# Kernel tuning notes

Hardware: AMD Instinct MI355X
Metric: run time of the kernel (lower is better)

The kernel has to match this reference:

```python
import jax, jax.numpy as jnp
import numpy as np

N_NODES = 50000
N_EDGES = 800000
D_IN, D_HID, D_OUT = 96, 96, 48


def _gcn_conv(x, src, dst, W, b, num_nodes):
    """PyG GCNConv: h = x @ W; out[dst] += norm * h[src]; out += b.
    Symmetric normalization deg^{-1/2}[src] * deg^{-1/2}[dst], self-loops included
    (src/dst already contain self-loops)."""
    h = x @ W  # [N, d_out]
    deg = jax.ops.segment_sum(jnp.ones_like(dst, dtype=h.dtype), dst,
                              num_segments=num_nodes)  # in-degree incl. self-loop
    dinv = jnp.where(deg > 0, jax.lax.rsqrt(deg), 0.0)
    norm = dinv[src] * dinv[dst]  # [E+N]
    msgs = h[src] * norm[:, None]  # gather + scale (the memory-bound part)
    out = jax.ops.segment_sum(msgs, dst, num_segments=num_nodes)  # scatter-add
    return out + b


def setup_inputs() -> dict:
    key = jax.random.key(0)
    k1, k2, k3, k4 = jax.random.split(key, 4)
    x = jax.random.normal(k1, (N_NODES, D_IN), dtype=jnp.float32)
    edge_index = jax.random.randint(k2, (2, N_EDGES), 0, N_NODES, dtype=jnp.int64)
    # Glorot-ish init for weights, zero bias (matches GCNConv defaults)
    W1 = jax.random.normal(k3, (D_IN, D_HID), dtype=jnp.float32) / np.sqrt(D_IN)
    b1 = jnp.zeros((D_HID,), dtype=jnp.float32)
    W2 = jax.random.normal(k4, (D_HID, D_OUT), dtype=jnp.float32) / np.sqrt(D_HID)
    b2 = jnp.zeros((D_OUT,), dtype=jnp.float32)
    return {"x": x, "edge_index": edge_index, "W1": W1, "b1": b1, "W2": W2, "b2": b2}


def reference(x, edge_index, W1, b1, W2, b2):
    num_nodes = x.shape[0]
    loops = jnp.arange(num_nodes, dtype=edge_index.dtype)
    src = jnp.concatenate([edge_index[0], loops])  # add self-loops
    dst = jnp.concatenate([edge_index[1], loops])
    h = _gcn_conv(x, src, dst, W1, b1, num_nodes)
    h = jax.nn.relu(h)
    # dropout p=0.5 is identity in eval mode (self.training=False)
    out = _gcn_conv(h, src, dst, W2, b2, num_nodes)
    return out
```

## Files before the change

kernel.cpp:

```cpp
#include <hip/hip_runtime.h>
#include <hip/hip_bf16.h>


constexpr int NN = 50000;
constexpr int NE = 800000;
constexpr int DI = 96;
constexpr int DH = 96;
constexpr int DO = 48;

constexpr int BK_SHIFT = 6;
constexpr int NBK      = (NN + 63) >> 6;
constexpr int BK_CAP   = 2048;

constexpr int NCHUNK = 256;
constexpr int CH     = (NE + NCHUNK - 1) / NCHUNK;

typedef unsigned short us8 __attribute__((ext_vector_type(8)));

__device__ __forceinline__ float bf2f(unsigned short u) {
    return __uint_as_float(((unsigned int)u) << 16);
}
__device__ __forceinline__ unsigned short f2bf(float f) {
    __hip_bfloat16 b = __float2bfloat16(f);
    return *reinterpret_cast<unsigned short*>(&b);
}


__global__ __launch_bounds__(256) void k_hist(const int* __restrict__ dst,
                                              int* __restrict__ C, int e) {
    __shared__ int hist[NBK];
    for (int i = threadIdx.x; i < NBK; i += 256) hist[i] = 0;
    __syncthreads();
    const int blk = blockIdx.x;
    const int beg = blk * CH, end = min(beg + CH, e);
    for (int i = beg + threadIdx.x; i < end; i += 256)
        atomicAdd(&hist[dst[i] >> BK_SHIFT], 1);
    __syncthreads();
    for (int b = threadIdx.x; b < NBK; b += 256)
        C[b * NCHUNK + blk] = hist[b];
}

__global__ __launch_bounds__(256) void k_rowscan(int* __restrict__ C,
                                                 int* __restrict__ totals,
                                                 int* __restrict__ row_ptr) {
    if (blockIdx.x == 0 && threadIdx.x == 0) row_ptr[NN] = NE;
    const int w    = threadIdx.x >> 6;
    const int lane = threadIdx.x & 63;
    const int r    = blockIdx.x * 4 + w;
    if (r >= NBK) return;
    int* row = C + r * NCHUNK;
    int v[4], s[4];
#pragma unroll
    for (int q = 0; q < 4; ++q) { v[q] = row[q * 64 + lane]; s[q] = v[q]; }
#pragma unroll
    for (int off = 1; off < 64; off <<= 1) {
#pragma unroll
        for (int q = 0; q < 4; ++q) {
            int y = __shfl_up(s[q], off);
            if (lane >= off) s[q] += y;
        }
    }
    int c0 = __shfl(s[0], 63);
    int c1 = __shfl(s[1], 63);
    int c2 = __shfl(s[2], 63);
    s[1] += c0;
    s[2] += c0 + c1;
    s[3] += c0 + c1 + c2;
#pragma unroll
    for (int q = 0; q < 4; ++q) row[q * 64 + lane] = s[q] - v[q];
    if (lane == 63) totals[r] = s[3];
}

__global__ __launch_bounds__(256) void k_scatter(const int* __restrict__ src,
                                                 const int* __restrict__ dst,
                                                 const int* __restrict__ C,
                                                 const int* __restrict__ totals,
                                                 int* __restrict__ bk_ptr,
                                                 unsigned* __restrict__ ebuf, int e) {
    __shared__ int bkL[NBK + 1];
    __shared__ int part[256];
    __shared__ int cur[NBK];
    const int t = threadIdx.x;

    int v[4];
    int s = 0;
    const int base = t * 4;
#pragma unroll
    for (int i = 0; i < 4; ++i) {
        int idx = base + i;
        v[i] = (idx < NBK) ? totals[idx] : 0;
        s += v[i];
    }
    part[t] = s;
    __syncthreads();
#pragma unroll
    for (int off = 1; off < 256; off <<= 1) {
        int x = part[t];
        int a = (t >= off) ? part[t - off] : 0;
        __syncthreads();
        part[t] = x + a;
        __syncthreads();
    }
    int run = part[t] - s;
#pragma unroll
    for (int i = 0; i < 4; ++i) {
        int idx = base + i;
        if (idx <= NBK) bkL[idx] = run;
        run += v[i];
    }
    __syncthreads();

    const int blk = blockIdx.x;
    for (int b = t; b < NBK; b += 256) cur[b] = bkL[b] + C[b * NCHUNK + blk];
    if (blk == 0)
        for (int i = t; i <= NBK; i += 256) bk_ptr[i] = bkL[i];
    __syncthreads();

    const int beg = blk * CH, end = min(beg + CH, e);
    for (int i = beg + t; i < end; i += 256) {
        int d = dst[i];
        int b = d >> BK_SHIFT;
        int pos = atomicAdd(&cur[b], 1);
        ebuf[pos] = ((unsigned)(d & 63) << 16) | (unsigned)src[i];
    }
}

__global__ __launch_bounds__(256) void k_bsort(const unsigned* __restrict__ ebuf,
                                               const int* __restrict__ bk_ptr,
                                               int* __restrict__ row_ptr,
                                               float* __restrict__ dinv,
                                               unsigned short* __restrict__ src16, int n) {
    __shared__ unsigned eL[BK_CAP];
    __shared__ unsigned short outL[BK_CAP];
    __shared__ int curL[64];
    __shared__ int baseL[64];

    const int b   = blockIdx.x;
    const int beg = bk_ptr[b];
    const int m   = bk_ptr[b + 1] - beg;
    const int t   = threadIdx.x;

    if (t < 64) curL[t] = 0;
    __syncthreads();

    for (int i = t; i < m; i += 256) {
        unsigned v = ebuf[beg + i];
        eL[i] = v;
        atomicAdd(&curL[v >> 16], 1);
    }
    __syncthreads();

    if (t < 64) {
        int c = curL[t];
        int x = c;
#pragma unroll
        for (int off = 1; off < 64; off <<= 1) {
            int y = __shfl_up(x, off);
            if (t >= off) x += y;
        }
        int excl = x - c;
        baseL[t] = excl;
        int d0 = (b << BK_SHIFT) + t;
        if (d0 < n) {
            row_ptr[d0] = beg + excl;
            dinv[d0]    = rsqrtf((float)(c + 1));
        }
    }
    __syncthreads();
    if (t < 64) curL[t] = baseL[t];
    __syncthreads();

    for (int i = t; i < m; i += 256) {
        unsigned v = eL[i];
        int p = atomicAdd(&curL[v >> 16], 1);
        outL[p] = (unsigned short)(v & 0xFFFFu);
    }
    __syncthreads();
    for (int i = t; i < m; i += 256) src16[beg + i] = outL[i];
}


__global__ __launch_bounds__(256) void k_gemm1(const float* __restrict__ X,
                                               const float* __restrict__ W,
                                               const float* __restrict__ dinv,
                                               unsigned short* __restrict__ Hsl, int n) {
    constexpr int ROWS = 64, P = 97;
    __shared__ float ws[DI * DH];
    __shared__ float xs[ROWS * P];
    unsigned short* hout = reinterpret_cast<unsigned short*>(xs);

    const int tid  = threadIdx.x;
    const int row0 = blockIdx.x * ROWS;

    for (int i = tid; i < DI * DH; i += 256) ws[i] = W[i];
    {
        const float4* Xv = reinterpret_cast<const float4*>(X + (size_t)row0 * DI);
        const int nv   = ROWS * DI / 4;
        const int maxv = ((n - row0) * DI) / 4;
        for (int i = tid; i < nv; i += 256) {
            float4 v = (i < maxv) ? Xv[i] : float4{0.f, 0.f, 0.f, 0.f};
            int r = i / 24, c = (i % 24) * 4;
            xs[r * P + c + 0] = v.x;
            xs[r * P + c + 1] = v.y;
            xs[r * P + c + 2] = v.z;
            xs[r * P + c + 3] = v.w;
        }
    }
    __syncthreads();

    const int cg = tid & 15, rg = tid >> 4;
    float acc[4][6] = {};
#pragma unroll 2
    for (int k = 0; k < DI; ++k) {
        float xv[4];
#pragma unroll
        for (int i = 0; i < 4; ++i) xv[i] = xs[(rg * 4 + i) * P + k];
#pragma unroll
        for (int j = 0; j < 6; ++j) {
            float wv = ws[k * DH + cg * 6 + j];
#pragma unroll
            for (int i = 0; i < 4; ++i) acc[i][j] += xv[i] * wv;
        }
    }
    __syncthreads();

#pragma unroll
    for (int i = 0; i < 4; ++i) {
        int row = row0 + rg * 4 + i;
        float dv = (row < n) ? dinv[row] : 0.f;
#pragma unroll
        for (int j = 0; j < 6; ++j)
            hout[(rg * 4 + i) * 96 + cg * 6 + j] = f2bf(acc[i][j] * dv);
    }
    __syncthreads();

    if (tid < 192) {
        int s = tid >> 6, r = tid & 63;
        int row = row0 + r;
        if (row < n) {
            const us8* srcp = reinterpret_cast<const us8*>(hout + r * 96 + s * 32);
            us8* dstp = reinterpret_cast<us8*>(Hsl + ((size_t)s * n + row) * 32);
#pragma unroll
            for (int q = 0; q < 4; ++q) dstp[q] = srcp[q];
        }
    }
}


__global__ __launch_bounds__(256) void k_gemm2(const unsigned short* __restrict__ A,
                                               const float* __restrict__ W,
                                               const float* __restrict__ dinv,
                                               unsigned short* __restrict__ H, int n) {
    constexpr int ROWS = 64, P = 98;
    __shared__ float ws[DH * DO];
    __shared__ unsigned short xs[ROWS * P];

    const int tid  = threadIdx.x;
    const int row0 = blockIdx.x * ROWS;

    for (int i = tid; i < DH * DO; i += 256) ws[i] = W[i];
    {
        const us8* Av = reinterpret_cast<const us8*>(A + (size_t)row0 * DH);
        const int nv   = ROWS * DH / 8;
        const int maxv = ((n - row0) * DH) / 8;
        for (int i = tid; i < nv; i += 256) {
            us8 v = (i < maxv) ? Av[i] : (us8)(0);
            int r = i / 12, c = (i % 12) * 8;
#pragma unroll
            for (int jj = 0; jj < 8; ++jj) xs[r * P + c + jj] = v[jj];
        }
    }
    __syncthreads();

    const int cg = tid & 15, rg = tid >> 4;
    float acc[4][3] = {};
#pragma unroll 2
    for (int k = 0; k < DH; ++k) {
        float xv[4];
#pragma unroll
        for (int i = 0; i < 4; ++i) xv[i] = bf2f(xs[(rg * 4 + i) * P + k]);
#pragma unroll
        for (int j = 0; j < 3; ++j) {
            float wv = ws[k * DO + cg * 3 + j];
#pragma unroll
            for (int i = 0; i < 4; ++i) acc[i][j] += xv[i] * wv;
        }
    }

#pragma unroll
    for (int i = 0; i < 4; ++i) {
        int row = row0 + rg * 4 + i;
        if (row < n) {
            float dv = dinv[row];
#pragma unroll
            for (int j = 0; j < 3; ++j)
                H[(size_t)row * DO + cg * 3 + j] = f2bf(acc[i][j] * dv);
        }
    }
}


__global__ __launch_bounds__(256) void k_agg_sl3(const unsigned short* __restrict__ hsl,
                                                 const float* __restrict__ dinv,
                                                 const int* __restrict__ row_ptr,
                                                 const unsigned short* __restrict__ src16,
                                                 const float* __restrict__ bias,
                                                 unsigned short* __restrict__ a1, int n) {
    const int v   = blockIdx.x & 7;
    const int s   = (v >= 6) ? (v - 6) : (v >= 3 ? v - 3 : v);
    const int rep = (v >= 6) ? 2 : (v >= 3 ? 1 : 0);
    const int R   = (s == 2) ? 2 : 3;
    const int cnt = (n + R - 1) / R;
    const int lo  = rep * cnt;
    const int hi  = min(lo + cnt, n);
    const int node = lo + ((int)(blockIdx.x >> 3) << 6) + ((int)threadIdx.x >> 2);
    if (node >= hi) return;
    const int g = threadIdx.x & 3;

    const us8* hs = reinterpret_cast<const us8*>(hsl + (size_t)s * n * 32);

    float accA[8], accB[8];
    {
        us8 hv = hs[(size_t)node * 4 + g];
#pragma unroll
        for (int j = 0; j < 8; ++j) { accA[j] = bf2f(hv[j]); accB[j] = 0.f; }
    }

    const int beg = row_ptr[node];
    const int end = row_ptr[node + 1];
    int k = beg;
    int kA = min((beg + 7) & ~7, end);
    for (; k < kA; ++k) {
        us8 vv = hs[(size_t)src16[k] * 4 + g];
#pragma unroll
        for (int j = 0; j < 8; ++j) accA[j] += bf2f(vv[j]);
    }
    for (; k + 8 <= end; k += 8) {
        us8 si = *reinterpret_cast<const us8*>(src16 + k);
        us8 v0 = hs[(size_t)si[0] * 4 + g];
        us8 v1 = hs[(size_t)si[1] * 4 + g];
        us8 v2 = hs[(size_t)si[2] * 4 + g];
        us8 v3 = hs[(size_t)si[3] * 4 + g];
        us8 v4 = hs[(size_t)si[4] * 4 + g];
        us8 v5 = hs[(size_t)si[5] * 4 + g];
        us8 v6 = hs[(size_t)si[6] * 4 + g];
        us8 v7 = hs[(size_t)si[7] * 4 + g];
#pragma unroll
        for (int j = 0; j < 8; ++j) {
            accA[j] += (bf2f(v0[j]) + bf2f(v1[j])) + (bf2f(v4[j]) + bf2f(v5[j]));
            accB[j] += (bf2f(v2[j]) + bf2f(v3[j])) + (bf2f(v6[j]) + bf2f(v7[j]));
        }
    }
    for (; k < end; ++k) {
        us8 vv = hs[(size_t)src16[k] * 4 + g];
#pragma unroll
        for (int j = 0; j < 8; ++j) accB[j] += bf2f(vv[j]);
    }

    const float di = dinv[node];
    const float4* b4 = reinterpret_cast<const float4*>(bias);
    float4 b0 = b4[s * 8 + g * 2], b1 = b4[s * 8 + g * 2 + 1];
    float r[8];
#pragma unroll
    for (int j = 0; j < 8; ++j) r[j] = di * (accA[j] + accB[j]);
    r[0] += b0.x; r[1] += b0.y; r[2] += b0.z; r[3] += b0.w;
    r[4] += b1.x; r[5] += b1.y; r[6] += b1.z; r[7] += b1.w;
    us8 o;
#pragma unroll
    for (int j = 0; j < 8; ++j) o[j] = f2bf(fmaxf(r[j], 0.f));
    *reinterpret_cast<us8*>(a1 + (size_t)node * DH + s * 32 + g * 8) = o;
}


template<int D, bool RELU, bool OUTBF16>
__global__ __launch_bounds__(256) void k_agg_csr(const unsigned short* __restrict__ h,
                                                 const float* __restrict__ dinv,
                                                 const int* __restrict__ row_ptr,
                                                 const unsigned short* __restrict__ src16,
                                                 const float* __restrict__ bias,
                                                 void* __restrict__ outp, int n) {
    constexpr int G = D / 8;
    int t = blockIdx.x * blockDim.x + threadIdx.x;
    if (t >= n * G) return;
    const int node = t / G;
    const int g    = t % G;

    const us8* h8 = reinterpret_cast<const us8*>(h);

    float accA[8], accB[8];
    {
        us8 hv = h8[(size_t)node * G + g];
#pragma unroll
        for (int j = 0; j < 8; ++j) { accA[j] = bf2f(hv[j]); accB[j] = 0.f; }
    }

    const int beg = row_ptr[node];
    const int end = row_ptr[node + 1];
    int k = beg;
    int kA = min((beg + 7) & ~7, end);
    for (; k < kA; ++k) {
        us8 vv = h8[(size_t)src16[k] * G + g];
#pragma unroll
        for (int j = 0; j < 8; ++j) accA[j] += bf2f(vv[j]);
    }
    for (; k + 8 <= end; k += 8) {
        us8 si = *reinterpret_cast<const us8*>(src16 + k);
        us8 v0 = h8[(size_t)si[0] * G + g];
        us8 v1 = h8[(size_t)si[1] * G + g];
        us8 v2 = h8[(size_t)si[2] * G + g];
        us8 v3 = h8[(size_t)si[3] * G + g];
        us8 v4 = h8[(size_t)si[4] * G + g];
        us8 v5 = h8[(size_t)si[5] * G + g];
        us8 v6 = h8[(size_t)si[6] * G + g];
        us8 v7 = h8[(size_t)si[7] * G + g];
#pragma unroll
        for (int j = 0; j < 8; ++j) {
            accA[j] += (bf2f(v0[j]) + bf2f(v1[j])) + (bf2f(v4[j]) + bf2f(v5[j]));
            accB[j] += (bf2f(v2[j]) + bf2f(v3[j])) + (bf2f(v6[j]) + bf2f(v7[j]));
        }
    }
    for (; k < end; ++k) {
        us8 vv = h8[(size_t)src16[k] * G + g];
#pragma unroll
        for (int j = 0; j < 8; ++j) accB[j] += bf2f(vv[j]);
    }

    const float di = dinv[node];
    const float4* b4 = reinterpret_cast<const float4*>(bias);
    float4 b0 = b4[g * 2], b1 = b4[g * 2 + 1];
    float r[8];
#pragma unroll
    for (int j = 0; j < 8; ++j) r[j] = di * (accA[j] + accB[j]);
    r[0] += b0.x; r[1] += b0.y; r[2] += b0.z; r[3] += b0.w;
    r[4] += b1.x; r[5] += b1.y; r[6] += b1.z; r[7] += b1.w;
    if (RELU) {
#pragma unroll
        for (int j = 0; j < 8; ++j) r[j] = fmaxf(r[j], 0.f);
    }
    if (OUTBF16) {
        us8 o;
#pragma unroll
        for (int j = 0; j < 8; ++j) o[j] = f2bf(r[j]);
        reinterpret_cast<us8*>((unsigned short*)outp)[(size_t)node * G + g] = o;
    } else {
        float4* o4 = reinterpret_cast<float4*>((float*)outp + (size_t)node * D + g * 8);
        o4[0] = float4{r[0], r[1], r[2], r[3]};
        o4[1] = float4{r[4], r[5], r[6], r[7]};
    }
}


extern "C" void kernel_launch(void* const* d_in, const int* in_sizes, int n_in,
                              void* d_out, int out_size, void* d_ws, size_t ws_size,
                              hipStream_t stream) {
    const float* x   = (const float*)d_in[0];
    const int*   ei  = (const int*)d_in[1];
    const float* W1  = (const float*)d_in[2];
    const float* b1  = (const float*)d_in[3];
    const float* W2  = (const float*)d_in[4];
    const float* b2  = (const float*)d_in[5];
    float*       out = (float*)d_out;

    const int* srcv = ei;
    const int* dstv = ei + NE;

    char* p = (char*)d_ws;
    float*          dinv  = (float*)p;           p += (size_t)NN * 4;
    unsigned short* a1    = (unsigned short*)p;  p += (size_t)NN * DH * 2;
    unsigned short* h1sl  = (unsigned short*)p;  p += (size_t)3 * NN * 32 * 2;
    int*      row_ptr     = (int*)p;             p += (size_t)(NN + 16) * 4;
    unsigned short* src16 = (unsigned short*)p;  p += (size_t)NE * 2;
    unsigned* ebuf        = (unsigned*)p;        p += (size_t)NE * 4;
    int*      Cm          = (int*)p;             p += (size_t)NBK * NCHUNK * 4;
    int*      totals      = (int*)p;             p += (size_t)NBK * 4;
    int*      bk_ptr      = (int*)p;             p += (size_t)(NBK + 1) * 4;

    const int B = 256;

    k_hist<<<NCHUNK, B, 0, stream>>>(dstv, Cm, NE);
    k_rowscan<<<(NBK + 3) / 4, B, 0, stream>>>(Cm, totals, row_ptr);
    k_scatter<<<NCHUNK, B, 0, stream>>>(srcv, dstv, Cm, totals, bk_ptr, ebuf, NE);
    k_bsort<<<NBK, B, 0, stream>>>(ebuf, bk_ptr, row_ptr, dinv, src16, NN);

    k_gemm1<<<(NN + 63) / 64, B, 0, stream>>>(x, W1, dinv, h1sl, NN);
    {
        const int NCH = ((NN + 1) / 2 + 63) / 64;
        k_agg_sl3<<<NCH * 8, B, 0, stream>>>(h1sl, dinv, row_ptr, src16, b1, a1, NN);
    }

    unsigned short* h2 = h1sl;
    k_gemm2<<<(NN + 63) / 64, B, 0, stream>>>(a1, W2, dinv, h2, NN);
    {
        int total = NN * (DO / 8);
        k_agg_csr<DO, false, false><<<(total + B - 1) / B, B, 0, stream>>>(
            h2, dinv, row_ptr, src16, b2, out, NN);
    }
}
```

Before: 132.6 us.

## Replace sliced layer-1 aggregation with row-major CSR aggregation and staged GEMM stores

Drops the three-slice column-split layout for the layer-1 hidden features and the dedicated k_agg_sl3 kernel. Layer 1 now uses the generic k_agg_csr template on a plain row-major bf16 array. k_gemm2 now stages its output in shared memory and writes it out with contiguous 16-byte vector stores instead of scattered 2-byte stores. The slicing existed to improve cache locality of the random gathers (each slice of 50000x32 bf16 is smaller), so dropping it trades that locality for simpler, fully contiguous row access.

```diff
diff --git a/kernel.cpp b/kernel.cpp
--- a/kernel.cpp
+++ b/kernel.cpp
@@ -183,7 +183,7 @@
 __global__ __launch_bounds__(256) void k_gemm1(const float* __restrict__ X,
                                                const float* __restrict__ W,
                                                const float* __restrict__ dinv,
-                                               unsigned short* __restrict__ Hsl, int n) {
+                                               unsigned short* __restrict__ H, int n) {
     constexpr int ROWS = 64, P = 97;
     __shared__ float ws[DI * DH];
     __shared__ float xs[ROWS * P];
@@ -234,15 +234,12 @@
     }
     __syncthreads();
 
-    if (tid < 192) {
-        int s = tid >> 6, r = tid & 63;
-        int row = row0 + r;
-        if (row < n) {
-            const us8* srcp = reinterpret_cast<const us8*>(hout + r * 96 + s * 32);
-            us8* dstp = reinterpret_cast<us8*>(Hsl + ((size_t)s * n + row) * 32);
-#pragma unroll
-            for (int q = 0; q < 4; ++q) dstp[q] = srcp[q];
-        }
+    {
+        const us8* ho8 = reinterpret_cast<const us8*>(hout);
+        us8* H8 = reinterpret_cast<us8*>(H + (size_t)row0 * DH);
+        const int nv   = ROWS * DH / 8;
+        const int maxv = ((n - row0) * DH) / 8;
+        for (int i = tid; i < nv && i < maxv; i += 256) H8[i] = ho8[i];
     }
 }
 
@@ -286,89 +283,26 @@
             for (int i = 0; i < 4; ++i) acc[i][j] += xv[i] * wv;
         }
     }
-
+    __syncthreads();
+
+    unsigned short* hout = xs;
 #pragma unroll
     for (int i = 0; i < 4; ++i) {
         int row = row0 + rg * 4 + i;
-        if (row < n) {
-            float dv = dinv[row];
-#pragma unroll
-            for (int j = 0; j < 3; ++j)
-                H[(size_t)row * DO + cg * 3 + j] = f2bf(acc[i][j] * dv);
-        }
-    }
-}
-
-
-__global__ __launch_bounds__(256) void k_agg_sl3(const unsigned short* __restrict__ hsl,
-                                                 const float* __restrict__ dinv,
-                                                 const int* __restrict__ row_ptr,
-                                                 const unsigned short* __restrict__ src16,
-                                                 const float* __restrict__ bias,
-                                                 unsigned short* __restrict__ a1, int n) {
-    const int v   = blockIdx.x & 7;
-    const int s   = (v >= 6) ? (v - 6) : (v >= 3 ? v - 3 : v);
-    const int rep = (v >= 6) ? 2 : (v >= 3 ? 1 : 0);
-    const int R   = (s == 2) ? 2 : 3;
-    const int cnt = (n + R - 1) / R;
-    const int lo  = rep * cnt;
-    const int hi  = min(lo + cnt, n);
-    const int node = lo + ((int)(blockIdx.x >> 3) << 6) + ((int)threadIdx.x >> 2);
-    if (node >= hi) return;
-    const int g = threadIdx.x & 3;
-
-    const us8* hs = reinterpret_cast<const us8*>(hsl + (size_t)s * n * 32);
-
-    float accA[8], accB[8];
-    {
-        us8 hv = hs[(size_t)node * 4 + g];
-#pragma unroll
-        for (int j = 0; j < 8; ++j) { accA[j] = bf2f(hv[j]); accB[j] = 0.f; }
-    }
-
-    const int beg = row_ptr[node];
-    const int end = row_ptr[node + 1];
-    int k = beg;
-    int kA = min((beg + 7) & ~7, end);
-    for (; k < kA; ++k) {
-        us8 vv = hs[(size_t)src16[k] * 4 + g];
-#pragma unroll
-        for (int j = 0; j < 8; ++j) accA[j] += bf2f(vv[j]);
-    }
-    for (; k + 8 <= end; k += 8) {
-        us8 si = *reinterpret_cast<const us8*>(src16 + k);
-        us8 v0 = hs[(size_t)si[0] * 4 + g];
-        us8 v1 = hs[(size_t)si[1] * 4 + g];
-        us8 v2 = hs[(size_t)si[2] * 4 + g];
-        us8 v3 = hs[(size_t)si[3] * 4 + g];
-        us8 v4 = hs[(size_t)si[4] * 4 + g];
-        us8 v5 = hs[(size_t)si[5] * 4 + g];
-        us8 v6 = hs[(size_t)si[6] * 4 + g];
-        us8 v7 = hs[(size_t)si[7] * 4 + g];
-#pragma unroll
-        for (int j = 0; j < 8; ++j) {
-            accA[j] += (bf2f(v0[j]) + bf2f(v1[j])) + (bf2f(v4[j]) + bf2f(v5[j]));
-            accB[j] += (bf2f(v2[j]) + bf2f(v3[j])) + (bf2f(v6[j]) + bf2f(v7[j]));
-        }
-    }
-    for (; k < end; ++k) {
-        us8 vv = hs[(size_t)src16[k] * 4 + g];
-#pragma unroll
-        for (int j = 0; j < 8; ++j) accB[j] += bf2f(vv[j]);
-    }
-
-    const float di = dinv[node];
-    const float4* b4 = reinterpret_cast<const float4*>(bias);
-    float4 b0 = b4[s * 8 + g * 2], b1 = b4[s * 8 + g * 2 + 1];
-    float r[8];
-#pragma unroll
-    for (int j = 0; j < 8; ++j) r[j] = di * (accA[j] + accB[j]);
-    r[0] += b0.x; r[1] += b0.y; r[2] += b0.z; r[3] += b0.w;
-    r[4] += b1.x; r[5] += b1.y; r[6] += b1.z; r[7] += b1.w;
-    us8 o;
-#pragma unroll
-    for (int j = 0; j < 8; ++j) o[j] = f2bf(fmaxf(r[j], 0.f));
-    *reinterpret_cast<us8*>(a1 + (size_t)node * DH + s * 32 + g * 8) = o;
+        float dv = (row < n) ? dinv[row] : 0.f;
+#pragma unroll
+        for (int j = 0; j < 3; ++j)
+            hout[(rg * 4 + i) * 48 + cg * 3 + j] = f2bf(acc[i][j] * dv);
+    }
+    __syncthreads();
+
+    {
+        const us8* ho8 = reinterpret_cast<const us8*>(hout);
+        us8* H8 = reinterpret_cast<us8*>(H + (size_t)row0 * DO);
+        const int nv   = ROWS * DO / 8;
+        const int maxv = ((n - row0) * DO) / 8;
+        for (int i = tid; i < nv && i < maxv; i += 256) H8[i] = ho8[i];
+    }
 }
 
 
@@ -467,7 +401,7 @@
     char* p = (char*)d_ws;
     float*          dinv  = (float*)p;           p += (size_t)NN * 4;
     unsigned short* a1    = (unsigned short*)p;  p += (size_t)NN * DH * 2;
-    unsigned short* h1sl  = (unsigned short*)p;  p += (size_t)3 * NN * 32 * 2;
+    unsigned short* h1    = (unsigned short*)p;  p += (size_t)NN * DH * 2;
     int*      row_ptr     = (int*)p;             p += (size_t)(NN + 16) * 4;
     unsigned short* src16 = (unsigned short*)p;  p += (size_t)NE * 2;
     unsigned* ebuf        = (unsigned*)p;        p += (size_t)NE * 4;
@@ -482,13 +416,14 @@
     k_scatter<<<NCHUNK, B, 0, stream>>>(srcv, dstv, Cm, totals, bk_ptr, ebuf, NE);
     k_bsort<<<NBK, B, 0, stream>>>(ebuf, bk_ptr, row_ptr, dinv, src16, NN);
 
-    k_gemm1<<<(NN + 63) / 64, B, 0, stream>>>(x, W1, dinv, h1sl, NN);
-    {
-        const int NCH = ((NN + 1) / 2 + 63) / 64;
-        k_agg_sl3<<<NCH * 8, B, 0, stream>>>(h1sl, dinv, row_ptr, src16, b1, a1, NN);
-    }
-
-    unsigned short* h2 = h1sl;
+    k_gemm1<<<(NN + 63) / 64, B, 0, stream>>>(x, W1, dinv, h1, NN);
+    {
+        int total = NN * (DH / 8);
+        k_agg_csr<DH, true, true><<<(total + B - 1) / B, B, 0, stream>>>(
+            h1, dinv, row_ptr, src16, b1, a1, NN);
+    }
+
+    unsigned short* h2 = h1;
     k_gemm2<<<(NN + 63) / 64, B, 0, stream>>>(a1, W2, dinv, h2, NN);
     {
         int total = NN * (DO / 8);
```

Result: faster. 125.8 us (-5.1%).
